# Kernel tuning notes

Measured on AMD Instinct MI355X. Metric: run time of the kernel, lower is better.

The kernel has to match this reference:

```python
import jax, jax.numpy as jnp
import numpy as np
import math

N_NODES = 50000
N_EDGES = 800000
D_IN = 128
HID = 128  # layer dims: 128 -> 128 -> 64 -> 32


def _glorot(key, fan_in, fan_out):
    lim = math.sqrt(6.0 / (fan_in + fan_out))
    return jax.random.uniform(key, (fan_in, fan_out), jnp.float32, -lim, lim)


def setup_inputs() -> dict:
    key = jax.random.key(0)
    ks = jax.random.split(key, 9)
    x = jax.random.normal(ks[0], (N_NODES, D_IN), dtype=jnp.float32)
    edge_index = jax.random.randint(ks[1], (2, N_EDGES), 0, N_NODES, dtype=jnp.int64)
    edge_attr = jax.random.uniform(ks[2], (N_EDGES,), dtype=jnp.float32)
    return {
        "x": x,
        "edge_index": edge_index,
        "edge_attr": edge_attr,
        "W1": _glorot(ks[3], D_IN, HID),      "b1": jnp.zeros((HID,), jnp.float32),
        "W2": _glorot(ks[4], HID, HID // 2),  "b2": jnp.zeros((HID // 2,), jnp.float32),
        "W3": _glorot(ks[5], HID // 2, HID // 4), "b3": jnp.zeros((HID // 4,), jnp.float32),
    }


def _gcn_conv(h, W, b, src, dst, norm, n_nodes):
    # GCNConv: linear transform, then normalized scatter-add aggregation, then bias
    h = h @ W                                   # [N, F_out]
    msg = h[src] * norm[:, None]                # gather + scale, [E', F_out]
    out = jax.ops.segment_sum(msg, dst, num_segments=n_nodes)  # scatter-add
    return out + b


def reference(x, edge_index, edge_attr, W1, b1, W2, b2, W3, b3):
    n = x.shape[0]
    # add self-loops with weight 1.0 (PyG GCNConv default)
    loop = jnp.arange(n, dtype=edge_index.dtype)
    src = jnp.concatenate([edge_index[0], loop])
    dst = jnp.concatenate([edge_index[1], loop])
    w = jnp.concatenate([edge_attr, jnp.ones((n,), edge_attr.dtype)])
    # symmetric normalization: D^{-1/2} A_hat D^{-1/2}
    deg = jax.ops.segment_sum(w, dst, num_segments=n)
    dinv = jnp.where(deg > 0, jax.lax.rsqrt(jnp.maximum(deg, 1e-30)), 0.0)
    norm = dinv[src] * w * dinv[dst]            # [E + N]

    h = jax.nn.relu(_gcn_conv(x, W1, b1, src, dst, norm, n))
    # dropout is identity in eval mode
    h = jax.nn.relu(_gcn_conv(h, W2, b2, src, dst, norm, n))
    h = _gcn_conv(h, W3, b3, src, dst, norm, n)
    return h
```

## Files before the change

### kernel.cpp

```cpp
#include <hip/hip_runtime.h>
#include <hip/hip_bf16.h>

#define BLK 256
#define SCAT_NB 512
#define BIN_SHIFT 8
#define STAGE_CAP 6144

typedef unsigned short ushort_t;
typedef unsigned int uint_t;
typedef unsigned long long ull_t;
typedef __attribute__((ext_vector_type(8))) short bf16x8;
typedef __attribute__((ext_vector_type(4))) float f32x4;

static __device__ __forceinline__ float bf2f(ushort_t u) {
    return __uint_as_float((uint_t)u << 16);
}
static __device__ __forceinline__ ushort_t f2bf(float f) {
    __hip_bfloat16 h = __float2bfloat16(f);
    return *reinterpret_cast<ushort_t*>(&h);
}



__global__ __launch_bounds__(256) void k_pre(const int* __restrict__ eidx,
                                             int* __restrict__ bcnt,
                                             int nbins, int epb, int E,
                                             const float* __restrict__ W1, ushort_t* __restrict__ Wt1,
                                             const float* __restrict__ W2, ushort_t* __restrict__ Wt2,
                                             const float* __restrict__ W3, ushort_t* __restrict__ Wt3) {
    const int b = blockIdx.x;
    const int t = threadIdx.x;
    if (b < SCAT_NB) {
        __shared__ int h[256];
        h[t] = 0;
        __syncthreads();
        const int base = b * epb;
        const int lim  = min(base + epb, E);
        for (int e = base + t; e < lim; e += 256)
            atomicAdd(&h[eidx[E + e] >> BIN_SHIFT], 1);
        __syncthreads();
        if (t < nbins) bcnt[(size_t)t * SCAT_NB + b] = h[t];
    } else {
        int j = (b - SCAT_NB) * 256 + t;
        if (j < 128 * 128) {
            int r = j / 128, c = j % 128;
            Wt1[(size_t)c * 128 + r] = f2bf(W1[j]);
        } else if (j < 128 * 128 + 128 * 64) {
            j -= 128 * 128;
            int r = j / 64, c = j % 64;
            Wt2[(size_t)c * 128 + r] = f2bf(W2[j]);
        } else if (j < 128 * 128 + 128 * 64 + 64 * 32) {
            j -= 128 * 128 + 128 * 64;
            int r = j / 32, c = j % 32;
            Wt3[(size_t)c * 64 + r] = f2bf(W3[j]);
        }
    }
}


__global__ __launch_bounds__(256) void k_scan1(const int* __restrict__ cnt,
                                               int* rowptr, int* bsum, int n) {
    __shared__ int tile[256];
    const int t = threadIdx.x;
    const int i = blockIdx.x * 256 + t;
    int v = (i < n) ? cnt[i] : 0;
    tile[t] = v;
    __syncthreads();
    for (int off = 1; off < 256; off <<= 1) {
        int x = (t >= off) ? tile[t - off] : 0;
        __syncthreads();
        tile[t] += x;
        __syncthreads();
    }
    if (i < n) rowptr[i] = tile[t] - v;
    if (t == 255) bsum[blockIdx.x] = tile[255];
}

__global__ __launch_bounds__(256) void k_scan2x(int* a, int n) {
    __shared__ int tile[256];
    __shared__ int carry_s;
    const int t = threadIdx.x;
    if (t == 0) carry_s = 0;
    __syncthreads();
    for (int base = 0; base < n; base += 256) {
        int i = base + t;
        int v = (i < n) ? a[i] : 0;
        tile[t] = v;
        __syncthreads();
        for (int off = 1; off < 256; off <<= 1) {
            int x = (t >= off) ? tile[t - off] : 0;
            __syncthreads();
            tile[t] += x;
            __syncthreads();
        }
        int carry = carry_s;
        if (i < n) a[i] = carry + tile[t] - v;
        __syncthreads();
        if (t == 255) carry_s = carry + tile[255];
        __syncthreads();
    }
}



__global__ __launch_bounds__(256) void k_bin_scatter(const int* __restrict__ eidx,
                                                     const float* __restrict__ ea,
                                                     const int* __restrict__ ebofs,
                                                     const int* __restrict__ bsumB,
                                                     uint2* __restrict__ binned,
                                                     int nbins, int epb, int E) {
    __shared__ int h[256];
    __shared__ int lofs[256];
    const int t = threadIdx.x;
    h[t] = 0;
    if (t < nbins) {
        int idx = t * SCAT_NB + blockIdx.x;
        lofs[t] = ebofs[idx] + bsumB[idx >> 8];
    }
    __syncthreads();
    const int base = blockIdx.x * epb;
    const int lim  = min(base + epb, E);
    for (int e = base + t; e < lim; e += 256) {
        int s = eidx[e];
        int d = eidx[E + e];
        float w = ea[e];
        int bin = d >> BIN_SHIFT;
        int r = atomicAdd(&h[bin], 1);
        int pos = lofs[bin] + r;
        binned[pos] = make_uint2(((uint_t)s << 8) | (uint_t)(d & 255), __float_as_uint(w));
    }
}


__global__ __launch_bounds__(256) void k_bin_finish(const uint2* __restrict__ binned,
                                                    const int* __restrict__ ebofs,
                                                    const int* __restrict__ bsumB,
                                                    float* __restrict__ dinv,
                                                    int* __restrict__ rowptr,
                                                    int* __restrict__ csr_src,
                                                    float* __restrict__ csr_val,
                                                    int nbins, int N, int E) {
    __shared__ uint2 stage[STAGE_CAP];
    __shared__ ull_t hs[256];
    __shared__ int   sc[256];
    __shared__ int   rp[256];
    __shared__ float dl[256];
    __shared__ int   c2[256];
    const int t = threadIdx.x;
    const int b = blockIdx.x;
    hs[t] = 0ull;
    c2[t] = 0;
    __syncthreads();
    const int i0 = b * SCAT_NB;
    const int start = ebofs[i0] + bsumB[i0 >> 8];
    int end = E;
    if (b + 1 < nbins) {
        int i1 = (b + 1) * SCAT_NB;
        end = ebofs[i1] + bsumB[i1 >> 8];
    }
    const int cnt = end - start;
    const bool fits = (cnt <= STAGE_CAP);

    if (fits) {
        for (int i = t; i < cnt; i += 256) {
            uint2 p = binned[start + i];
            stage[i] = p;
            atomicAdd(&hs[p.x & 255],
                      (1ull << 40) | (ull_t)(__uint_as_float(p.y) * 4294967296.0f));
        }
    } else {
        for (int i = start + t; i < end; i += 256) {
            uint2 p = binned[i];
            atomicAdd(&hs[p.x & 255],
                      (1ull << 40) | (ull_t)(__uint_as_float(p.y) * 4294967296.0f));
        }
    }
    __syncthreads();

    int v = (int)(hs[t] >> 40);
    sc[t] = v;
    __syncthreads();
    for (int off = 1; off < 256; off <<= 1) {
        int x = (t >= off) ? sc[t - off] : 0;
        __syncthreads();
        sc[t] += x;
        __syncthreads();
    }
    {
        ull_t s = hs[t];
        float dg = 1.0f + (float)(s & ((1ull << 40) - 1)) * (1.0f / 4294967296.0f);
        float di = rsqrtf(dg);
        dl[t] = di;
        rp[t] = start + sc[t] - v;
        const int node = (b << BIN_SHIFT) + t;
        if (node < N) {
            dinv[node]   = di;
            rowptr[node] = rp[t];
        }
        if (b == 0 && t == 0) rowptr[N] = E;
    }
    __syncthreads();

    if (fits) {
        for (int i = t; i < cnt; i += 256) {
            uint2 p = stage[i];
            int d8 = p.x & 255;
            int r = atomicAdd(&c2[d8], 1);
            int pos = rp[d8] + r;
            csr_src[pos] = (int)(p.x >> 8);
            csr_val[pos] = __uint_as_float(p.y) * dl[d8];
        }
    } else {
        for (int i = start + t; i < end; i += 256) {
            uint2 p = binned[i];
            int d8 = p.x & 255;
            int r = atomicAdd(&c2[d8], 1);
            int pos = rp[d8] + r;
            csr_src[pos] = (int)(p.x >> 8);
            csr_val[pos] = __uint_as_float(p.y) * dl[d8];
        }
    }
}


template <int FIN, int FOUT, bool AF32>
__global__ __launch_bounds__(256) void k_gemm_mfma(const void* __restrict__ Av,
                                                   const ushort_t* __restrict__ Wt,
                                                   const float* __restrict__ dinv,
                                                   ushort_t* __restrict__ C, int n) {
    constexpr int NT = FOUT / 16;
    constexpr int NK = FIN / 32;
    const int wave = threadIdx.x >> 6;
    const int lane = threadIdx.x & 63;
    const int r0 = (blockIdx.x * 4 + wave) * 32;
    if (r0 >= n) return;

    const int l15 = lane & 15;
    const int kg  = lane >> 4;
    const int arow0 = min(r0 + l15, n - 1);
    const int arow1 = min(r0 + 16 + l15, n - 1);

    f32x4 acc0[NT], acc1[NT];
#pragma unroll
    for (int c = 0; c < NT; ++c) { acc0[c] = (f32x4)(0.0f); acc1[c] = (f32x4)(0.0f); }

    const ushort_t* Bp = Wt + (size_t)l15 * FIN + kg * 8;

#pragma unroll 1
    for (int ks = 0; ks < NK; ++ks) {
        bf16x8 a0, a1;
        if (AF32) {
            const float* A = (const float*)Av;
            const float* p0 = A + (size_t)arow0 * FIN + kg * 8 + ks * 32;
            const float* p1 = A + (size_t)arow1 * FIN + kg * 8 + ks * 32;
            float4 u0 = *(const float4*)p0, u1 = *(const float4*)(p0 + 4);
            float4 w0 = *(const float4*)p1, w1 = *(const float4*)(p1 + 4);
            a0[0] = (short)f2bf(u0.x); a0[1] = (short)f2bf(u0.y);
            a0[2] = (short)f2bf(u0.z); a0[3] = (short)f2bf(u0.w);
            a0[4] = (short)f2bf(u1.x); a0[5] = (short)f2bf(u1.y);
            a0[6] = (short)f2bf(u1.z); a0[7] = (short)f2bf(u1.w);
            a1[0] = (short)f2bf(w0.x); a1[1] = (short)f2bf(w0.y);
            a1[2] = (short)f2bf(w0.z); a1[3] = (short)f2bf(w0.w);
            a1[4] = (short)f2bf(w1.x); a1[5] = (short)f2bf(w1.y);
            a1[6] = (short)f2bf(w1.z); a1[7] = (short)f2bf(w1.w);
        } else {
            const ushort_t* A = (const ushort_t*)Av;
            a0 = *(const bf16x8*)(A + (size_t)arow0 * FIN + kg * 8 + ks * 32);
            a1 = *(const bf16x8*)(A + (size_t)arow1 * FIN + kg * 8 + ks * 32);
        }
#pragma unroll
        for (int c = 0; c < NT; ++c) {
            bf16x8 bfr = *(const bf16x8*)(Bp + (size_t)c * 16 * FIN + ks * 32);
            acc0[c] = __builtin_amdgcn_mfma_f32_16x16x32_bf16(a0, bfr, acc0[c], 0, 0, 0);
            acc1[c] = __builtin_amdgcn_mfma_f32_16x16x32_bf16(a1, bfr, acc1[c], 0, 0, 0);
        }
    }

#pragma unroll
    for (int g = 0; g < 2; ++g) {
        const int rbase = r0 + g * 16 + kg * 4;
#pragma unroll
        for (int j = 0; j < 4; ++j) {
            int row = rbase + j;
            if (row < n) {
                float dscale = dinv[row];
#pragma unroll
                for (int c = 0; c < NT; ++c) {
                    float val = (g == 0) ? acc0[c][j] : acc1[c][j];
                    C[(size_t)row * FOUT + c * 16 + l15] = f2bf(val * dscale);
                }
            }
        }
    }
}


template <int FOUT, bool RELU, bool OBF16>
__global__ __launch_bounds__(256) void k_agg(const ushort_t* __restrict__ H,
                                             const float* __restrict__ dinv,
                                             const int* __restrict__ rowptr,
                                             const int* __restrict__ csr_src,
                                             const float* __restrict__ csr_val,
                                             const float* __restrict__ bias,
                                             void* __restrict__ outv, int n) {
    constexpr int LPN = FOUT / 4;
    constexpr int NPW = 64 / LPN;
    const int wave = threadIdx.x >> 6;
    const int lane = threadIdx.x & 63;
    const int sub  = lane / LPN;
    const int f4   = lane % LPN;
    const int node = (blockIdx.x * 4 + wave) * NPW + sub;
    if (node >= n) return;

    const ushort_t* __restrict__ Hf = H + 4 * f4;

    const float sn = dinv[node];
    ushort4 hv = *(const ushort4*)(Hf + (size_t)node * FOUT);
    float a0 = sn * bf2f(hv.x);
    float a1 = sn * bf2f(hv.y);
    float a2 = sn * bf2f(hv.z);
    float a3 = sn * bf2f(hv.w);

    const int e0 = rowptr[node], e1 = rowptr[node + 1];
    int e = e0;
    for (; e + 8 <= e1; e += 8) {
        int   s0 = csr_src[e+0], s1 = csr_src[e+1], s2 = csr_src[e+2], s3 = csr_src[e+3];
        int   s4 = csr_src[e+4], s5 = csr_src[e+5], s6 = csr_src[e+6], s7 = csr_src[e+7];
        float v0 = csr_val[e+0], v1 = csr_val[e+1], v2 = csr_val[e+2], v3 = csr_val[e+3];
        float v4 = csr_val[e+4], v5 = csr_val[e+5], v6 = csr_val[e+6], v7 = csr_val[e+7];
        ushort4 m0 = *(const ushort4*)(Hf + (size_t)s0 * FOUT);
        ushort4 m1 = *(const ushort4*)(Hf + (size_t)s1 * FOUT);
        ushort4 m2 = *(const ushort4*)(Hf + (size_t)s2 * FOUT);
        ushort4 m3 = *(const ushort4*)(Hf + (size_t)s3 * FOUT);
        ushort4 m4 = *(const ushort4*)(Hf + (size_t)s4 * FOUT);
        ushort4 m5 = *(const ushort4*)(Hf + (size_t)s5 * FOUT);
        ushort4 m6 = *(const ushort4*)(Hf + (size_t)s6 * FOUT);
        ushort4 m7 = *(const ushort4*)(Hf + (size_t)s7 * FOUT);
        a0 += v0 * bf2f(m0.x); a1 += v0 * bf2f(m0.y); a2 += v0 * bf2f(m0.z); a3 += v0 * bf2f(m0.w);
        a0 += v1 * bf2f(m1.x); a1 += v1 * bf2f(m1.y); a2 += v1 * bf2f(m1.z); a3 += v1 * bf2f(m1.w);
        a0 += v2 * bf2f(m2.x); a1 += v2 * bf2f(m2.y); a2 += v2 * bf2f(m2.z); a3 += v2 * bf2f(m2.w);
        a0 += v3 * bf2f(m3.x); a1 += v3 * bf2f(m3.y); a2 += v3 * bf2f(m3.z); a3 += v3 * bf2f(m3.w);
        a0 += v4 * bf2f(m4.x); a1 += v4 * bf2f(m4.y); a2 += v4 * bf2f(m4.z); a3 += v4 * bf2f(m4.w);
        a0 += v5 * bf2f(m5.x); a1 += v5 * bf2f(m5.y); a2 += v5 * bf2f(m5.z); a3 += v5 * bf2f(m5.w);
        a0 += v6 * bf2f(m6.x); a1 += v6 * bf2f(m6.y); a2 += v6 * bf2f(m6.z); a3 += v6 * bf2f(m6.w);
        a0 += v7 * bf2f(m7.x); a1 += v7 * bf2f(m7.y); a2 += v7 * bf2f(m7.z); a3 += v7 * bf2f(m7.w);
    }
    for (; e + 2 <= e1; e += 2) {
        int   s0 = csr_src[e+0], s1 = csr_src[e+1];
        float v0 = csr_val[e+0], v1 = csr_val[e+1];
        ushort4 m0 = *(const ushort4*)(Hf + (size_t)s0 * FOUT);
        ushort4 m1 = *(const ushort4*)(Hf + (size_t)s1 * FOUT);
        a0 += v0 * bf2f(m0.x); a1 += v0 * bf2f(m0.y); a2 += v0 * bf2f(m0.z); a3 += v0 * bf2f(m0.w);
        a0 += v1 * bf2f(m1.x); a1 += v1 * bf2f(m1.y); a2 += v1 * bf2f(m1.z); a3 += v1 * bf2f(m1.w);
    }
    if (e < e1) {
        int   s0 = csr_src[e];
        float v0 = csr_val[e];
        ushort4 m0 = *(const ushort4*)(Hf + (size_t)s0 * FOUT);
        a0 += v0 * bf2f(m0.x); a1 += v0 * bf2f(m0.y); a2 += v0 * bf2f(m0.z); a3 += v0 * bf2f(m0.w);
    }

    float4 bv = *(const float4*)(bias + 4 * f4);
    a0 += bv.x; a1 += bv.y; a2 += bv.z; a3 += bv.w;
    if (RELU) {
        a0 = fmaxf(a0, 0.f); a1 = fmaxf(a1, 0.f);
        a2 = fmaxf(a2, 0.f); a3 = fmaxf(a3, 0.f);
    }
    if (OBF16) {
        ushort4 o = make_ushort4(f2bf(a0), f2bf(a1), f2bf(a2), f2bf(a3));
        *(ushort4*)((ushort_t*)outv + (size_t)node * FOUT + 4 * f4) = o;
    } else {
        *(float4*)((float*)outv + (size_t)node * FOUT + 4 * f4) = make_float4(a0, a1, a2, a3);
    }
}


extern "C" void kernel_launch(void* const* d_in, const int* in_sizes, int n_in,
                              void* d_out, int out_size, void* d_ws, size_t ws_size,
                              hipStream_t stream) {
    const float* x    = (const float*)d_in[0];
    const int*   eidx = (const int*)d_in[1];
    const float* ea   = (const float*)d_in[2];
    const float* W1   = (const float*)d_in[3];
    const float* b1   = (const float*)d_in[4];
    const float* W2   = (const float*)d_in[5];
    const float* b2   = (const float*)d_in[6];
    const float* W3   = (const float*)d_in[7];
    const float* b3   = (const float*)d_in[8];

    const int N = in_sizes[0] / 128;
    const int E = in_sizes[2];

    const int nbins = (N + 255) >> BIN_SHIFT;
    const int epb   = (E + SCAT_NB - 1) / SCAT_NB;
    const int nbc   = nbins * SCAT_NB;
    const int gBC   = (nbc + BLK - 1) / BLK;

    char*  base = (char*)d_ws;
    size_t off  = 0;
    auto carve = [&](size_t nbytes) -> void* {
        void* p = base + off;
        off = (off + nbytes + 255) & ~(size_t)255;
        return p;
    };
    int*   bcnt      = (int*)  carve((size_t)nbc * 4);
    int*   ebofs     = (int*)  carve((size_t)nbc * 4);
    int*   bsumB     = (int*)  carve((size_t)512 * 4);
    uint2* binned    = (uint2*)carve((size_t)E * 8);
    float* dinv      = (float*)carve((size_t)N * 4);
    int*   rowptr    = (int*)  carve((size_t)(N + 1) * 4);
    int*   csr_src   = (int*)  carve((size_t)E * 4);
    float* csr_val   = (float*)carve((size_t)E * 4);
    ushort_t* bufA   = (ushort_t*)carve((size_t)N * 128 * 2);
    ushort_t* bufB   = (ushort_t*)carve((size_t)N * 128 * 2);
    ushort_t* Wt1    = (ushort_t*)carve((size_t)128 * 128 * 2);
    ushort_t* Wt2    = (ushort_t*)carve((size_t)64 * 128 * 2);
    ushort_t* Wt3    = (ushort_t*)carve((size_t)32 * 64 * 2);
    (void)ws_size;

    const int wtot = 128 * 128 + 128 * 64 + 64 * 32;
    const int gPre = SCAT_NB + (wtot + 255) / 256;
    const int gR = (N + 127) / 128;

    k_pre<<<gPre, BLK, 0, stream>>>(eidx, bcnt, nbins, epb, E, W1, Wt1, W2, Wt2, W3, Wt3);
    k_scan1<<<gBC, BLK, 0, stream>>>(bcnt, ebofs, bsumB, nbc);
    k_scan2x<<<1, BLK, 0, stream>>>(bsumB, gBC);
    k_bin_scatter<<<SCAT_NB, BLK, 0, stream>>>(eidx, ea, ebofs, bsumB, binned, nbins, epb, E);
    k_bin_finish<<<nbins, BLK, 0, stream>>>(binned, ebofs, bsumB, dinv, rowptr,
                                            csr_src, csr_val, nbins, N, E);

    k_gemm_mfma<128, 128, true><<<gR, BLK, 0, stream>>>(x, Wt1, dinv, bufA, N);
    k_agg<128, true, true><<<(N + 7) / 8, BLK, 0, stream>>>(bufA, dinv, rowptr, csr_src, csr_val, b1, bufB, N);

    k_gemm_mfma<128, 64, false><<<gR, BLK, 0, stream>>>(bufB, Wt2, dinv, bufA, N);
    k_agg<64, true, true><<<(N + 15) / 16, BLK, 0, stream>>>(bufA, dinv, rowptr, csr_src, csr_val, b2, bufB, N);

    k_gemm_mfma<64, 32, false><<<gR, BLK, 0, stream>>>(bufB, Wt3, dinv, bufA, N);
    k_agg<32, false, false><<<(N + 31) / 32, BLK, 0, stream>>>(bufA, dinv, rowptr, csr_src, csr_val, b3, d_out, N);
}
```

Measured before the change: 142.1 us.

## Fuse aggregation with next-layer GEMM through shared-memory tile

Layer-1 and layer-2 aggregation are each fused with the following layer's MFMA GEMM. Each block aggregates 32 nodes into a bf16 LDS tile, applies bias and ReLU, then multiplies that tile by the next weight matrix. This removes two kernel launches and the global write and reread of the intermediate activations. The cost is fewer, smaller blocks of 32 nodes, an added __syncthreads, and only 2*NT MFMA tiles spread over 4 waves, so GEMM-phase utilization may be low.

```diff
diff --git a/kernel.cpp b/kernel.cpp
--- a/kernel.cpp
+++ b/kernel.cpp
@@ -223,119 +223,26 @@
 }
 
 
-template <int FIN, int FOUT, bool AF32>
-__global__ __launch_bounds__(256) void k_gemm_mfma(const void* __restrict__ Av,
-                                                   const ushort_t* __restrict__ Wt,
-                                                   const float* __restrict__ dinv,
-                                                   ushort_t* __restrict__ C, int n) {
-    constexpr int NT = FOUT / 16;
-    constexpr int NK = FIN / 32;
-    const int wave = threadIdx.x >> 6;
-    const int lane = threadIdx.x & 63;
-    const int r0 = (blockIdx.x * 4 + wave) * 32;
-    if (r0 >= n) return;
-
-    const int l15 = lane & 15;
-    const int kg  = lane >> 4;
-    const int arow0 = min(r0 + l15, n - 1);
-    const int arow1 = min(r0 + 16 + l15, n - 1);
-
-    f32x4 acc0[NT], acc1[NT];
-#pragma unroll
-    for (int c = 0; c < NT; ++c) { acc0[c] = (f32x4)(0.0f); acc1[c] = (f32x4)(0.0f); }
-
-    const ushort_t* Bp = Wt + (size_t)l15 * FIN + kg * 8;
-
-#pragma unroll 1
-    for (int ks = 0; ks < NK; ++ks) {
-        bf16x8 a0, a1;
-        if (AF32) {
-            const float* A = (const float*)Av;
-            const float* p0 = A + (size_t)arow0 * FIN + kg * 8 + ks * 32;
-            const float* p1 = A + (size_t)arow1 * FIN + kg * 8 + ks * 32;
-            float4 u0 = *(const float4*)p0, u1 = *(const float4*)(p0 + 4);
-            float4 w0 = *(const float4*)p1, w1 = *(const float4*)(p1 + 4);
-            a0[0] = (short)f2bf(u0.x); a0[1] = (short)f2bf(u0.y);
-            a0[2] = (short)f2bf(u0.z); a0[3] = (short)f2bf(u0.w);
-            a0[4] = (short)f2bf(u1.x); a0[5] = (short)f2bf(u1.y);
-            a0[6] = (short)f2bf(u1.z); a0[7] = (short)f2bf(u1.w);
-            a1[0] = (short)f2bf(w0.x); a1[1] = (short)f2bf(w0.y);
-            a1[2] = (short)f2bf(w0.z); a1[3] = (short)f2bf(w0.w);
-            a1[4] = (short)f2bf(w1.x); a1[5] = (short)f2bf(w1.y);
-            a1[6] = (short)f2bf(w1.z); a1[7] = (short)f2bf(w1.w);
-        } else {
-            const ushort_t* A = (const ushort_t*)Av;
-            a0 = *(const bf16x8*)(A + (size_t)arow0 * FIN + kg * 8 + ks * 32);
-            a1 = *(const bf16x8*)(A + (size_t)arow1 * FIN + kg * 8 + ks * 32);
-        }
-#pragma unroll
-        for (int c = 0; c < NT; ++c) {
-            bf16x8 bfr = *(const bf16x8*)(Bp + (size_t)c * 16 * FIN + ks * 32);
-            acc0[c] = __builtin_amdgcn_mfma_f32_16x16x32_bf16(a0, bfr, acc0[c], 0, 0, 0);
-            acc1[c] = __builtin_amdgcn_mfma_f32_16x16x32_bf16(a1, bfr, acc1[c], 0, 0, 0);
-        }
-    }
-
-#pragma unroll
-    for (int g = 0; g < 2; ++g) {
-        const int rbase = r0 + g * 16 + kg * 4;
-#pragma unroll
-        for (int j = 0; j < 4; ++j) {
-            int row = rbase + j;
-            if (row < n) {
-                float dscale = dinv[row];
-#pragma unroll
-                for (int c = 0; c < NT; ++c) {
-                    float val = (g == 0) ? acc0[c][j] : acc1[c][j];
-                    C[(size_t)row * FOUT + c * 16 + l15] = f2bf(val * dscale);
-                }
-            }
-        }
-    }
-}
-
-
-template <int FOUT, bool RELU, bool OBF16>
-__global__ __launch_bounds__(256) void k_agg(const ushort_t* __restrict__ H,
-                                             const float* __restrict__ dinv,
-                                             const int* __restrict__ rowptr,
-                                             const int* __restrict__ csr_src,
-                                             const float* __restrict__ csr_val,
-                                             const float* __restrict__ bias,
-                                             void* __restrict__ outv, int n) {
-    constexpr int LPN = FOUT / 4;
-    constexpr int NPW = 64 / LPN;
-    const int wave = threadIdx.x >> 6;
-    const int lane = threadIdx.x & 63;
-    const int sub  = lane / LPN;
-    const int f4   = lane % LPN;
-    const int node = (blockIdx.x * 4 + wave) * NPW + sub;
-    if (node >= n) return;
-
-    const ushort_t* __restrict__ Hf = H + 4 * f4;
-
-    const float sn = dinv[node];
-    ushort4 hv = *(const ushort4*)(Hf + (size_t)node * FOUT);
-    float a0 = sn * bf2f(hv.x);
-    float a1 = sn * bf2f(hv.y);
-    float a2 = sn * bf2f(hv.z);
-    float a3 = sn * bf2f(hv.w);
-
-    const int e0 = rowptr[node], e1 = rowptr[node + 1];
+template <int FIN>
+static __device__ __forceinline__ void agg_body(const ushort_t* __restrict__ Hf,
+                                                const int* __restrict__ csr_src,
+                                                const float* __restrict__ csr_val,
+                                                int e0, int e1,
+                                                float& a0, float& a1, float& a2, float& a3) {
     int e = e0;
     for (; e + 8 <= e1; e += 8) {
         int   s0 = csr_src[e+0], s1 = csr_src[e+1], s2 = csr_src[e+2], s3 = csr_src[e+3];
         int   s4 = csr_src[e+4], s5 = csr_src[e+5], s6 = csr_src[e+6], s7 = csr_src[e+7];
         float v0 = csr_val[e+0], v1 = csr_val[e+1], v2 = csr_val[e+2], v3 = csr_val[e+3];
         float v4 = csr_val[e+4], v5 = csr_val[e+5], v6 = csr_val[e+6], v7 = csr_val[e+7];
-        ushort4 m0 = *(const ushort4*)(Hf + (size_t)s0 * FOUT);
-        ushort4 m1 = *(const ushort4*)(Hf + (size_t)s1 * FOUT);
-        ushort4 m2 = *(const ushort4*)(Hf + (size_t)s2 * FOUT);
-        ushort4 m3 = *(const ushort4*)(Hf + (size_t)s3 * FOUT);
-        ushort4 m4 = *(const ushort4*)(Hf + (size_t)s4 * FOUT);
-        ushort4 m5 = *(const ushort4*)(Hf + (size_t)s5 * FOUT);
-        ushort4 m6 = *(const ushort4*)(Hf + (size_t)s6 * FOUT);
-        ushort4 m7 = *(const ushort4*)(Hf + (size_t)s7 * FOUT);
+        ushort4 m0 = *(const ushort4*)(Hf + (size_t)s0 * FIN);
+        ushort4 m1 = *(const ushort4*)(Hf + (size_t)s1 * FIN);
+        ushort4 m2 = *(const ushort4*)(Hf + (size_t)s2 * FIN);
+        ushort4 m3 = *(const ushort4*)(Hf + (size_t)s3 * FIN);
+        ushort4 m4 = *(const ushort4*)(Hf + (size_t)s4 * FIN);
+        ushort4 m5 = *(const ushort4*)(Hf + (size_t)s5 * FIN);
+        ushort4 m6 = *(const ushort4*)(Hf + (size_t)s6 * FIN);
+        ushort4 m7 = *(const ushort4*)(Hf + (size_t)s7 * FIN);
         a0 += v0 * bf2f(m0.x); a1 += v0 * bf2f(m0.y); a2 += v0 * bf2f(m0.z); a3 += v0 * bf2f(m0.w);
         a0 += v1 * bf2f(m1.x); a1 += v1 * bf2f(m1.y); a2 += v1 * bf2f(m1.z); a3 += v1 * bf2f(m1.w);
         a0 += v2 * bf2f(m2.x); a1 += v2 * bf2f(m2.y); a2 += v2 * bf2f(m2.z); a3 += v2 * bf2f(m2.w);
@@ -348,30 +255,184 @@
     for (; e + 2 <= e1; e += 2) {
         int   s0 = csr_src[e+0], s1 = csr_src[e+1];
         float v0 = csr_val[e+0], v1 = csr_val[e+1];
-        ushort4 m0 = *(const ushort4*)(Hf + (size_t)s0 * FOUT);
-        ushort4 m1 = *(const ushort4*)(Hf + (size_t)s1 * FOUT);
+        ushort4 m0 = *(const ushort4*)(Hf + (size_t)s0 * FIN);
+        ushort4 m1 = *(const ushort4*)(Hf + (size_t)s1 * FIN);
         a0 += v0 * bf2f(m0.x); a1 += v0 * bf2f(m0.y); a2 += v0 * bf2f(m0.z); a3 += v0 * bf2f(m0.w);
         a0 += v1 * bf2f(m1.x); a1 += v1 * bf2f(m1.y); a2 += v1 * bf2f(m1.z); a3 += v1 * bf2f(m1.w);
     }
     if (e < e1) {
         int   s0 = csr_src[e];
         float v0 = csr_val[e];
-        ushort4 m0 = *(const ushort4*)(Hf + (size_t)s0 * FOUT);
+        ushort4 m0 = *(const ushort4*)(Hf + (size_t)s0 * FIN);
         a0 += v0 * bf2f(m0.x); a1 += v0 * bf2f(m0.y); a2 += v0 * bf2f(m0.z); a3 += v0 * bf2f(m0.w);
     }
+}
+
+
+template <int FIN, int FOUT>
+__global__ __launch_bounds__(256) void k_agg_gemm(const ushort_t* __restrict__ H,
+                                                  const float* __restrict__ dinv,
+                                                  const int* __restrict__ rowptr,
+                                                  const int* __restrict__ csr_src,
+                                                  const float* __restrict__ csr_val,
+                                                  const float* __restrict__ bias,
+                                                  const ushort_t* __restrict__ Wt,
+                                                  ushort_t* __restrict__ C, int n) {
+    constexpr int PAD = 8;
+    __shared__ ushort_t Gs[32][FIN + PAD];
+    constexpr int LPN = FIN / 4;
+    constexpr int NPW = 64 / LPN;
+    constexpr int NPB = NPW * 4;
+    constexpr int NPASS = 32 / NPB;
+    constexpr int NT = FOUT / 16;
+    constexpr int NK = FIN / 32;
+
+    const int wave = threadIdx.x >> 6;
+    const int lane = threadIdx.x & 63;
+    const int r0 = blockIdx.x * 32;
+    const int sub = lane / LPN;
+    const int f4  = lane % LPN;
+    const ushort_t* __restrict__ Hf = H + 4 * f4;
+
+#pragma unroll
+    for (int p = 0; p < NPASS; ++p) {
+        const int nb = p * NPB + wave * NPW + sub;
+        const int node = r0 + nb;
+        float a0 = 0.f, a1 = 0.f, a2 = 0.f, a3 = 0.f;
+        if (node < n) {
+            const float sn = dinv[node];
+            ushort4 hv = *(const ushort4*)(Hf + (size_t)node * FIN);
+            a0 = sn * bf2f(hv.x); a1 = sn * bf2f(hv.y);
+            a2 = sn * bf2f(hv.z); a3 = sn * bf2f(hv.w);
+            agg_body<FIN>(Hf, csr_src, csr_val, rowptr[node], rowptr[node + 1], a0, a1, a2, a3);
+            float4 bv = *(const float4*)(bias + 4 * f4);
+            a0 = fmaxf(a0 + bv.x, 0.f); a1 = fmaxf(a1 + bv.y, 0.f);
+            a2 = fmaxf(a2 + bv.z, 0.f); a3 = fmaxf(a3 + bv.w, 0.f);
+        }
+        *(ushort4*)(&Gs[nb][4 * f4]) = make_ushort4(f2bf(a0), f2bf(a1), f2bf(a2), f2bf(a3));
+    }
+    __syncthreads();
+
+    const int l15 = lane & 15;
+    const int kg  = lane >> 4;
+    for (int item = wave; item < 2 * NT; item += 4) {
+        const int g  = item / NT;
+        const int ct = item % NT;
+        f32x4 acc = (f32x4)(0.0f);
+        const ushort_t* Bp = Wt + (size_t)(ct * 16 + l15) * FIN + kg * 8;
+        const int arow = g * 16 + l15;
+#pragma unroll
+        for (int ks = 0; ks < NK; ++ks) {
+            bf16x8 a = *(const bf16x8*)(&Gs[arow][kg * 8 + ks * 32]);
+            bf16x8 b = *(const bf16x8*)(Bp + ks * 32);
+            acc = __builtin_amdgcn_mfma_f32_16x16x32_bf16(a, b, acc, 0, 0, 0);
+        }
+        const int rbase = r0 + g * 16 + kg * 4;
+#pragma unroll
+        for (int j = 0; j < 4; ++j) {
+            int row = rbase + j;
+            if (row < n)
+                C[(size_t)row * FOUT + ct * 16 + l15] = f2bf(acc[j] * dinv[row]);
+        }
+    }
+}
+
+
+template <int FIN, int FOUT>
+__global__ __launch_bounds__(256) void k_gemm_f32(const float* __restrict__ A,
+                                                  const ushort_t* __restrict__ Wt,
+                                                  const float* __restrict__ dinv,
+                                                  ushort_t* __restrict__ C, int n) {
+    constexpr int NT = FOUT / 16;
+    constexpr int NK = FIN / 32;
+    const int wave = threadIdx.x >> 6;
+    const int lane = threadIdx.x & 63;
+    const int r0 = (blockIdx.x * 4 + wave) * 32;
+    if (r0 >= n) return;
+
+    const int l15 = lane & 15;
+    const int kg  = lane >> 4;
+    const int arow0 = min(r0 + l15, n - 1);
+    const int arow1 = min(r0 + 16 + l15, n - 1);
+
+    f32x4 acc0[NT], acc1[NT];
+#pragma unroll
+    for (int c = 0; c < NT; ++c) { acc0[c] = (f32x4)(0.0f); acc1[c] = (f32x4)(0.0f); }
+
+    const ushort_t* Bp = Wt + (size_t)l15 * FIN + kg * 8;
+
+#pragma unroll 1
+    for (int ks = 0; ks < NK; ++ks) {
+        bf16x8 a0, a1;
+        const float* p0 = A + (size_t)arow0 * FIN + kg * 8 + ks * 32;
+        const float* p1 = A + (size_t)arow1 * FIN + kg * 8 + ks * 32;
+        float4 u0 = *(const float4*)p0, u1 = *(const float4*)(p0 + 4);
+        float4 w0 = *(const float4*)p1, w1 = *(const float4*)(p1 + 4);
+        a0[0] = (short)f2bf(u0.x); a0[1] = (short)f2bf(u0.y);
+        a0[2] = (short)f2bf(u0.z); a0[3] = (short)f2bf(u0.w);
+        a0[4] = (short)f2bf(u1.x); a0[5] = (short)f2bf(u1.y);
+        a0[6] = (short)f2bf(u1.z); a0[7] = (short)f2bf(u1.w);
+        a1[0] = (short)f2bf(w0.x); a1[1] = (short)f2bf(w0.y);
+        a1[2] = (short)f2bf(w0.z); a1[3] = (short)f2bf(w0.w);
+        a1[4] = (short)f2bf(w1.x); a1[5] = (short)f2bf(w1.y);
+        a1[6] = (short)f2bf(w1.z); a1[7] = (short)f2bf(w1.w);
+#pragma unroll
+        for (int c = 0; c < NT; ++c) {
+            bf16x8 bfr = *(const bf16x8*)(Bp + (size_t)c * 16 * FIN + ks * 32);
+            acc0[c] = __builtin_amdgcn_mfma_f32_16x16x32_bf16(a0, bfr, acc0[c], 0, 0, 0);
+            acc1[c] = __builtin_amdgcn_mfma_f32_16x16x32_bf16(a1, bfr, acc1[c], 0, 0, 0);
+        }
+    }
+
+#pragma unroll
+    for (int g = 0; g < 2; ++g) {
+        const int rbase = r0 + g * 16 + kg * 4;
+#pragma unroll
+        for (int j = 0; j < 4; ++j) {
+            int row = rbase + j;
+            if (row < n) {
+                float dscale = dinv[row];
+#pragma unroll
+                for (int c = 0; c < NT; ++c) {
+                    float val = (g == 0) ? acc0[c][j] : acc1[c][j];
+                    C[(size_t)row * FOUT + c * 16 + l15] = f2bf(val * dscale);
+                }
+            }
+        }
+    }
+}
+
+
+template <int FIN>
+__global__ __launch_bounds__(256) void k_agg_final(const ushort_t* __restrict__ H,
+                                                   const float* __restrict__ dinv,
+                                                   const int* __restrict__ rowptr,
+                                                   const int* __restrict__ csr_src,
+                                                   const float* __restrict__ csr_val,
+                                                   const float* __restrict__ bias,
+                                                   float* __restrict__ out, int n) {
+    constexpr int LPN = FIN / 4;
+    constexpr int NPW = 64 / LPN;
+    const int wave = threadIdx.x >> 6;
+    const int lane = threadIdx.x & 63;
+    const int sub  = lane / LPN;
+    const int f4   = lane % LPN;
+    const int node = (blockIdx.x * 4 + wave) * NPW + sub;
+    if (node >= n) return;
+
+    const ushort_t* __restrict__ Hf = H + 4 * f4;
+    const float sn = dinv[node];
+    ushort4 hv = *(const ushort4*)(Hf + (size_t)node * FIN);
+    float a0 = sn * bf2f(hv.x);
+    float a1 = sn * bf2f(hv.y);
+    float a2 = sn * bf2f(hv.z);
+    float a3 = sn * bf2f(hv.w);
+
+    agg_body<FIN>(Hf, csr_src, csr_val, rowptr[node], rowptr[node + 1], a0, a1, a2, a3);
 
     float4 bv = *(const float4*)(bias + 4 * f4);
     a0 += bv.x; a1 += bv.y; a2 += bv.z; a3 += bv.w;
-    if (RELU) {
-        a0 = fmaxf(a0, 0.f); a1 = fmaxf(a1, 0.f);
-        a2 = fmaxf(a2, 0.f); a3 = fmaxf(a3, 0.f);
-    }
-    if (OBF16) {
-        ushort4 o = make_ushort4(f2bf(a0), f2bf(a1), f2bf(a2), f2bf(a3));
-        *(ushort4*)((ushort_t*)outv + (size_t)node * FOUT + 4 * f4) = o;
-    } else {
-        *(float4*)((float*)outv + (size_t)node * FOUT + 4 * f4) = make_float4(a0, a1, a2, a3);
-    }
+    *(float4*)(out + (size_t)node * FIN + 4 * f4) = make_float4(a0, a1, a2, a3);
 }
 
 
@@ -412,7 +473,7 @@
     int*   csr_src   = (int*)  carve((size_t)E * 4);
     float* csr_val   = (float*)carve((size_t)E * 4);
     ushort_t* bufA   = (ushort_t*)carve((size_t)N * 128 * 2);
-    ushort_t* bufB   = (ushort_t*)carve((size_t)N * 128 * 2);
+    ushort_t* bufB   = (ushort_t*)carve((size_t)N * 64 * 2);
     ushort_t* Wt1    = (ushort_t*)carve((size_t)128 * 128 * 2);
     ushort_t* Wt2    = (ushort_t*)carve((size_t)64 * 128 * 2);
     ushort_t* Wt3    = (ushort_t*)carve((size_t)32 * 64 * 2);
@@ -420,7 +481,8 @@
 
     const int wtot = 128 * 128 + 128 * 64 + 64 * 32;
     const int gPre = SCAT_NB + (wtot + 255) / 256;
-    const int gR = (N + 127) / 128;
+    const int gR  = (N + 127) / 128;
+    const int gF  = (N + 31) / 32;
 
     k_pre<<<gPre, BLK, 0, stream>>>(eidx, bcnt, nbins, epb, E, W1, Wt1, W2, Wt2, W3, Wt3);
     k_scan1<<<gBC, BLK, 0, stream>>>(bcnt, ebofs, bsumB, nbc);
@@ -429,12 +491,14 @@
     k_bin_finish<<<nbins, BLK, 0, stream>>>(binned, ebofs, bsumB, dinv, rowptr,
                                             csr_src, csr_val, nbins, N, E);
 
-    k_gemm_mfma<128, 128, true><<<gR, BLK, 0, stream>>>(x, Wt1, dinv, bufA, N);
-    k_agg<128, true, true><<<(N + 7) / 8, BLK, 0, stream>>>(bufA, dinv, rowptr, csr_src, csr_val, b1, bufB, N);
-
-    k_gemm_mfma<128, 64, false><<<gR, BLK, 0, stream>>>(bufB, Wt2, dinv, bufA, N);
-    k_agg<64, true, true><<<(N + 15) / 16, BLK, 0, stream>>>(bufA, dinv, rowptr, csr_src, csr_val, b2, bufB, N);
-
-    k_gemm_mfma<64, 32, false><<<gR, BLK, 0, stream>>>(bufB, Wt3, dinv, bufA, N);
-    k_agg<32, false, false><<<(N + 31) / 32, BLK, 0, stream>>>(bufA, dinv, rowptr, csr_src, csr_val, b3, d_out, N);
-}
+    k_gemm_f32<128, 128><<<gR, BLK, 0, stream>>>(x, Wt1, dinv, bufA, N);
+
+    k_agg_gemm<128, 64><<<gF, BLK, 0, stream>>>(bufA, dinv, rowptr, csr_src, csr_val,
+                                                b1, Wt2, bufB, N);
+
+    k_agg_gemm<64, 32><<<gF, BLK, 0, stream>>>(bufB, dinv, rowptr, csr_src, csr_val,
+                                               b2, Wt3, bufA, N);
+
+    k_agg_final<32><<<(N + 31) / 32, BLK, 0, stream>>>(bufA, dinv, rowptr, csr_src, csr_val,
+                                                       b3, (float*)d_out, N);
+}
```

Result: faster. 136.8 us (-3.7%).
